# Optimization experiments

Hardware: AMD Instinct MI355X
Metric: run time of the kernel (lower is better)

## Reference

```python
import jax, jax.numpy as jnp
import numpy as np

# Constants derived from quantiles=[0.1..0.9] (deciles), df = 9.
QUANTILES = jnp.array([0.1, 0.2, 0.3, 0.4, 0.5, 0.6, 0.7, 0.8, 0.9], dtype=jnp.float32)
# scipy.stats.norm.ppf(quantiles), cast to float32 as in the torch module
Z_SCORES = jnp.array([-1.2815516, -0.8416212, -0.5244005, -0.2533471, 0.0,
                      0.2533471, 0.5244005, 0.8416212, 1.2815516], dtype=jnp.float32)
# expected bin probabilities: q0, diffs, 1-q_last -> all 0.1 for deciles
EXPECTED_PCT = jnp.full((10,), 0.1, dtype=jnp.float32)
# chi2.ppf(1 - p, df=9) for p in QUANTILES (precomputed with scipy offline)
CRIT = jnp.array([14.683657, 12.242145, 10.656372, 9.413640, 8.342832,
                  7.357034, 6.393306, 5.380053, 4.168159], dtype=jnp.float32)
MAX_CRIT = 14.683657
SHARPNESS = 100.0  # sigmoid steepness for the soft histogram


def setup_inputs() -> dict:
    key = jax.random.key(0)
    x = jax.random.normal(key, (16777216,), dtype=jnp.float32)
    return {"x": x}


def reference(x):
    n = x.shape[0]
    mean = x.mean()
    std = jnp.std(x, ddof=1)  # torch.std uses Bessel's correction
    z = (x - mean) / std  # [n]
    # soft cumulative counts at each quantile threshold: [K]
    cum = jax.nn.sigmoid(SHARPNESS * (Z_SCORES[:, None] - z[None, :])).sum(axis=1)
    # bin counts: first cum, consecutive diffs, remainder n - last cum -> [K+1]
    actual = jnp.concatenate([cum[:1], jnp.diff(cum),
                              jnp.asarray(n, z.dtype)[None] - cum[-1:]])
    expected = n * EXPECTED_PCT
    chi2_stat = jnp.sum((actual - expected) ** 2 / (expected + 1e-7))
    # differentiable interpolation of p-value
    w = jax.nn.softmax(-jnp.abs(chi2_stat - CRIT))
    p_value_estimate = 1.0 - jnp.sum(w * QUANTILES)
    excess = jax.nn.relu((chi2_stat - MAX_CRIT) / 100.0)
    return p_value_estimate + excess
```

## Files before the change

kernel.cpp:

```cpp
#include <hip/hip_runtime.h>
#include <math.h>


#if __has_builtin(__builtin_amdgcn_exp2f)
#define EXP2F(x) __builtin_amdgcn_exp2f(x)
#else
#define EXP2F(x) exp2f(x)
#endif
#if __has_builtin(__builtin_amdgcn_rcpf)
#define RCPF(x) __builtin_amdgcn_rcpf(x)
#else
#define RCPF(x) (1.0f / (x))
#endif

#define NBLK 256
#define ABLOCK 1024
#define NBINS 8192

static __device__ __forceinline__ double wave_reduce_d(double v) {
#pragma unroll
    for (int off = 32; off > 0; off >>= 1) v += __shfl_down(v, off);
    return v;
}

__device__ __constant__ double d_ZS[9] = {
    -1.2815516, -0.8416212, -0.5244005, -0.2533471, 0.0,
    0.2533471,  0.5244005,  0.8416212,  1.2815516};

__device__ void epilogue(const double* cum, float* out, int n) {
    const double CRIT[9] = {14.683657, 12.242145, 10.656372, 9.413640, 8.342832,
                            7.357034,  6.393306,  5.380053,  4.168159};
    const double nd = (double)n;
    double actual[10];
    actual[0] = cum[0];
#pragma unroll
    for (int k = 1; k < 9; ++k) actual[k] = cum[k] - cum[k - 1];
    actual[9] = nd - cum[8];
    const double expected = nd * (double)0.1f;
    const double denom = expected + 1e-7;
    double chi2 = 0.0;
#pragma unroll
    for (int j = 0; j < 10; ++j) {
        double d = actual[j] - expected;
        chi2 += d * d / denom;
    }
    double dneg[9], m = -1e300;
#pragma unroll
    for (int k = 0; k < 9; ++k) {
        dneg[k] = -fabs(chi2 - CRIT[k]);
        if (dneg[k] > m) m = dneg[k];
    }
    double W = 0.0, PQ = 0.0;
#pragma unroll
    for (int k = 0; k < 9; ++k) {
        double w = exp(dneg[k] - m);
        W += w;
        PQ += w * (0.1 * (double)(k + 1));
    }
    double p = 1.0 - PQ / W;
    double excess = (chi2 - 14.683657) / 100.0;
    if (excess < 0.0) excess = 0.0;
    out[0] = (float)(p + excess);
}

__global__ __launch_bounds__(ABLOCK) void init_kernel(unsigned int* __restrict__ H,
                                                      unsigned int* __restrict__ ticket) {
    const int t = blockIdx.x * ABLOCK + threadIdx.x;
    if (t < NBINS) H[t] = 0u;
    if (t == 0) *ticket = 0u;
}

__global__ __launch_bounds__(ABLOCK) void fused_kernel(
    const float* __restrict__ x, double* __restrict__ part1,
    unsigned int* __restrict__ H, unsigned int* __restrict__ ticket,
    float* __restrict__ out, int n) {
    __shared__ unsigned int hist[NBINS];
    __shared__ double smd[16][9];
    __shared__ double sMV[2];
    __shared__ int sLast;
    const int tx = threadIdx.x;
    const int lane = tx & 63, wid = tx >> 6;

#pragma unroll
    for (int j = 0; j < NBINS / ABLOCK; ++j) hist[tx + j * ABLOCK] = 0u;
    __syncthreads();

    float fs = 0.f, fss = 0.f;
    auto process = [&](float v) {
        fs += v;
        fss = fmaf(v, v, fss);
        int b = (int)fmaf(v, 512.0f, 4096.0f);
        b = b < 0 ? 0 : (b > NBINS - 1 ? NBINS - 1 : b);
        atomicAdd(&hist[b], 1u);
    };

    const int tid = blockIdx.x * ABLOCK + tx;
    const int nthreads = NBLK * ABLOCK;
    const int n4 = n >> 2;
    const float4* __restrict__ x4 = (const float4*)x;
    for (int i = tid; i < n4; i += nthreads) {
        float4 v = x4[i];
        process(v.x); process(v.y); process(v.z); process(v.w);
    }
    if (blockIdx.x == 0 && tx == 0) {
        for (int j = n4 << 2; j < n; ++j) process(x[j]);
    }
    __syncthreads();

#pragma unroll
    for (int j = 0; j < NBINS / ABLOCK; ++j) {
        const int jj = (j + (int)blockIdx.x) & (NBINS / ABLOCK - 1);
        const int b = tx + jj * ABLOCK;
        const unsigned int h = hist[b];
        if (h) atomicAdd(&H[b], h);
    }

    double s = wave_reduce_d((double)fs);
    double ss = wave_reduce_d((double)fss);
    if (lane == 0) { smd[wid][0] = s; smd[wid][1] = ss; }
    __syncthreads();
    if (tx == 0) {
        double ts = 0.0, tss = 0.0;
#pragma unroll
        for (int w = 0; w < 16; ++w) { ts += smd[w][0]; tss += smd[w][1]; }
        __hip_atomic_store(&part1[2 * blockIdx.x], ts, __ATOMIC_RELAXED,
                           __HIP_MEMORY_SCOPE_AGENT);
        __hip_atomic_store(&part1[2 * blockIdx.x + 1], tss, __ATOMIC_RELAXED,
                           __HIP_MEMORY_SCOPE_AGENT);
    }

    __syncthreads();
    if (tx == 0) {
        __threadfence();
        const unsigned int prev = __hip_atomic_fetch_add(
            ticket, 1u, __ATOMIC_ACQ_REL, __HIP_MEMORY_SCOPE_AGENT);
        sLast = (prev == (unsigned int)(NBLK - 1));
    }
    __syncthreads();
    if (!sLast) return;
    __threadfence();

    double ps = 0.0, pss = 0.0;
    if (tx < NBLK) {
        ps = __hip_atomic_load(&part1[2 * tx], __ATOMIC_RELAXED,
                               __HIP_MEMORY_SCOPE_AGENT);
        pss = __hip_atomic_load(&part1[2 * tx + 1], __ATOMIC_RELAXED,
                                __HIP_MEMORY_SCOPE_AGENT);
    }
    double rs = wave_reduce_d(ps);
    double rss = wave_reduce_d(pss);
    __syncthreads();
    if (lane == 0) { smd[wid][0] = rs; smd[wid][1] = rss; }
    __syncthreads();
    if (tx == 0) {
        double ts = 0.0, tss = 0.0;
#pragma unroll
        for (int w = 0; w < 16; ++w) { ts += smd[w][0]; tss += smd[w][1]; }
        const double nd = (double)n;
        const double mean = ts / nd;
        const double var = (tss - ts * ts / nd) / (nd - 1.0);
        sMV[0] = mean;
        sMV[1] = 1.0 / sqrt(var);
    }
    __syncthreads();
    const double mu = sMV[0], isig = sMV[1];
    const double Ld = 144.26950408889634;
    const double wz = (1.0 / 512.0) * isig;
    const double wz2_12 = wz * wz / 12.0;
    const double hgl = wz * 0.28867513459481287;

    double acc[9];
#pragma unroll
    for (int k = 0; k < 9; ++k) acc[k] = 0.0;

    for (int b = tx; b < NBINS; b += ABLOCK) {
        const unsigned int h = __hip_atomic_load(&H[b], __ATOMIC_RELAXED,
                                                 __HIP_MEMORY_SCOPE_AGENT);
        if (h == 0u) continue;
        const double dh = (double)h;
        const double c = (double)b * (1.0 / 512.0) + (0.5 / 512.0 - 8.0);
        const double zc = (c - mu) * isig;
        const double zctr = zc - zc * wz2_12;
        const double z1 = zctr - hgl, z2 = zctr + hgl;
#pragma unroll
        for (int k = 0; k < 9; ++k) {
            const float t1 = EXP2F((float)(Ld * (z1 - d_ZS[k])));
            const float t2 = EXP2F((float)(Ld * (z2 - d_ZS[k])));
            const double sg =
                0.5 * ((double)RCPF(1.0f + t1) + (double)RCPF(1.0f + t2));
            acc[k] += dh * sg;
        }
    }

    __syncthreads();
#pragma unroll
    for (int k = 0; k < 9; ++k) {
        double r = wave_reduce_d(acc[k]);
        if (lane == 0) smd[wid][k] = r;
    }
    __syncthreads();
    if (tx == 0) {
        double cum[9];
#pragma unroll
        for (int k = 0; k < 9; ++k) {
            double t = 0.0;
#pragma unroll
            for (int w = 0; w < 16; ++w) t += smd[w][k];
            cum[k] = t;
        }
        epilogue(cum, out, n);
    }
}

extern "C" void kernel_launch(void* const* d_in, const int* in_sizes, int n_in,
                              void* d_out, int out_size, void* d_ws, size_t ws_size,
                              hipStream_t stream) {
    const float* x = (const float*)d_in[0];
    const int n = in_sizes[0];
    double* part1 = (double*)d_ws;
    unsigned int* H = (unsigned int*)(part1 + 512);
    unsigned int* ticket = H + NBINS;

    init_kernel<<<8, ABLOCK, 0, stream>>>(H, ticket);
    fused_kernel<<<NBLK, ABLOCK, 0, stream>>>(x, part1, H, ticket,
                                              (float*)d_out, n);
}
```

Before: 121.9 us.

## Replace global histogram merge with cooperative grid sync and per-block sigmoid evaluation

Launches the kernel cooperatively and uses a grid-wide sync after the mean/variance partials, so every block can evaluate the soft-sigmoid sums on its own shared-memory histogram. This removes the atomic merge into a global histogram, the separate init kernel, and the single last-block tail that evaluated all bins alone. Per-block cumulative sums are written to a second partial buffer and reduced by the last block via a ticket, which is reset inside the kernel. In exchange, every block repeats the bin loop over all 8192 bins, and a cooperative launch and grid barrier are added.

```diff
diff --git a/kernel.cpp b/kernel.cpp
--- a/kernel.cpp
+++ b/kernel.cpp
@@ -1,5 +1,8 @@
 #include <hip/hip_runtime.h>
+#include <hip/hip_cooperative_groups.h>
 #include <math.h>
+
+namespace cg = cooperative_groups;
 
 
 #if __has_builtin(__builtin_amdgcn_exp2f)
@@ -63,23 +66,20 @@
     out[0] = (float)(p + excess);
 }
 
-__global__ __launch_bounds__(ABLOCK) void init_kernel(unsigned int* __restrict__ H,
-                                                      unsigned int* __restrict__ ticket) {
-    const int t = blockIdx.x * ABLOCK + threadIdx.x;
-    if (t < NBINS) H[t] = 0u;
-    if (t == 0) *ticket = 0u;
-}
-
 __global__ __launch_bounds__(ABLOCK) void fused_kernel(
     const float* __restrict__ x, double* __restrict__ part1,
-    unsigned int* __restrict__ H, unsigned int* __restrict__ ticket,
+    double* __restrict__ part2, unsigned int* __restrict__ ticket,
     float* __restrict__ out, int n) {
+    cg::grid_group grid = cg::this_grid();
     __shared__ unsigned int hist[NBINS];
     __shared__ double smd[16][9];
     __shared__ double sMV[2];
     __shared__ int sLast;
     const int tx = threadIdx.x;
     const int lane = tx & 63, wid = tx >> 6;
+
+    if (blockIdx.x == 0 && tx == 0)
+        __hip_atomic_store(ticket, 0u, __ATOMIC_RELAXED, __HIP_MEMORY_SCOPE_AGENT);
 
 #pragma unroll
     for (int j = 0; j < NBINS / ABLOCK; ++j) hist[tx + j * ABLOCK] = 0u;
@@ -107,14 +107,6 @@
     }
     __syncthreads();
 
-#pragma unroll
-    for (int j = 0; j < NBINS / ABLOCK; ++j) {
-        const int jj = (j + (int)blockIdx.x) & (NBINS / ABLOCK - 1);
-        const int b = tx + jj * ABLOCK;
-        const unsigned int h = hist[b];
-        if (h) atomicAdd(&H[b], h);
-    }
-
     double s = wave_reduce_d((double)fs);
     double ss = wave_reduce_d((double)fss);
     if (lane == 0) { smd[wid][0] = s; smd[wid][1] = ss; }
@@ -127,18 +119,10 @@
                            __HIP_MEMORY_SCOPE_AGENT);
         __hip_atomic_store(&part1[2 * blockIdx.x + 1], tss, __ATOMIC_RELAXED,
                            __HIP_MEMORY_SCOPE_AGENT);
-    }
-
-    __syncthreads();
-    if (tx == 0) {
         __threadfence();
-        const unsigned int prev = __hip_atomic_fetch_add(
-            ticket, 1u, __ATOMIC_ACQ_REL, __HIP_MEMORY_SCOPE_AGENT);
-        sLast = (prev == (unsigned int)(NBLK - 1));
-    }
-    __syncthreads();
-    if (!sLast) return;
-    __threadfence();
+    }
+
+    grid.sync();
 
     double ps = 0.0, pss = 0.0;
     if (tx < NBLK) {
@@ -174,8 +158,7 @@
     for (int k = 0; k < 9; ++k) acc[k] = 0.0;
 
     for (int b = tx; b < NBINS; b += ABLOCK) {
-        const unsigned int h = __hip_atomic_load(&H[b], __ATOMIC_RELAXED,
-                                                 __HIP_MEMORY_SCOPE_AGENT);
+        const unsigned int h = hist[b];
         if (h == 0u) continue;
         const double dh = (double)h;
         const double c = (double)b * (1.0 / 512.0) + (0.5 / 512.0 - 8.0);
@@ -200,6 +183,40 @@
     }
     __syncthreads();
     if (tx == 0) {
+#pragma unroll
+        for (int k = 0; k < 9; ++k) {
+            double t = 0.0;
+#pragma unroll
+            for (int w = 0; w < 16; ++w) t += smd[w][k];
+            __hip_atomic_store(&part2[blockIdx.x * 9 + k], t, __ATOMIC_RELAXED,
+                               __HIP_MEMORY_SCOPE_AGENT);
+        }
+        __threadfence();
+        const unsigned int prev = __hip_atomic_fetch_add(
+            ticket, 1u, __ATOMIC_ACQ_REL, __HIP_MEMORY_SCOPE_AGENT);
+        sLast = (prev == (unsigned int)(NBLK - 1));
+    }
+    __syncthreads();
+    if (!sLast) return;
+    __threadfence();
+
+    double v9[9];
+#pragma unroll
+    for (int k = 0; k < 9; ++k) v9[k] = 0.0;
+    if (tx < NBLK) {
+#pragma unroll
+        for (int k = 0; k < 9; ++k)
+            v9[k] = __hip_atomic_load(&part2[tx * 9 + k], __ATOMIC_RELAXED,
+                                      __HIP_MEMORY_SCOPE_AGENT);
+    }
+    __syncthreads();
+#pragma unroll
+    for (int k = 0; k < 9; ++k) {
+        double r = wave_reduce_d(v9[k]);
+        if (lane == 0) smd[wid][k] = r;
+    }
+    __syncthreads();
+    if (tx == 0) {
         double cum[9];
 #pragma unroll
         for (int k = 0; k < 9; ++k) {
@@ -216,12 +233,14 @@
                               void* d_out, int out_size, void* d_ws, size_t ws_size,
                               hipStream_t stream) {
     const float* x = (const float*)d_in[0];
-    const int n = in_sizes[0];
+    int n = in_sizes[0];
     double* part1 = (double*)d_ws;
-    unsigned int* H = (unsigned int*)(part1 + 512);
-    unsigned int* ticket = H + NBINS;
-
-    init_kernel<<<8, ABLOCK, 0, stream>>>(H, ticket);
-    fused_kernel<<<NBLK, ABLOCK, 0, stream>>>(x, part1, H, ticket,
-                                              (float*)d_out, n);
-}
+    double* part2 = part1 + 512;
+    unsigned int* ticket = (unsigned int*)(part2 + NBLK * 9);
+    float* outp = (float*)d_out;
+
+    void* kargs[] = {(void*)&x, (void*)&part1, (void*)&part2,
+                     (void*)&ticket, (void*)&outp, (void*)&n};
+    hipLaunchCooperativeKernel((void*)fused_kernel, dim3(NBLK), dim3(ABLOCK),
+                               kargs, 0u, stream);
+}
```

After: 166.3 us. 1.36x slower.

## Replicate global histogram, double block count, and batch loads per thread

Applied to the files above, without the earlier changes.

Doubles the grid to 512 blocks with a launch-bounds occupancy hint, and unrolls the streaming loop to issue four float4 loads before processing them. The global histogram is split into 8 replicas indexed by block to spread atomic contention, and the last block sums the replicas when reading. In exchange, init and the final reduction touch 8x more histogram memory, and the extra blocks add more shared-histogram flushes.

```diff
diff --git a/kernel.cpp b/kernel.cpp
--- a/kernel.cpp
+++ b/kernel.cpp
@@ -13,9 +13,10 @@
 #define RCPF(x) (1.0f / (x))
 #endif
 
-#define NBLK 256
+#define NBLK 512
 #define ABLOCK 1024
 #define NBINS 8192
+#define NREP 8
 
 static __device__ __forceinline__ double wave_reduce_d(double v) {
 #pragma unroll
@@ -66,11 +67,11 @@
 __global__ __launch_bounds__(ABLOCK) void init_kernel(unsigned int* __restrict__ H,
                                                       unsigned int* __restrict__ ticket) {
     const int t = blockIdx.x * ABLOCK + threadIdx.x;
-    if (t < NBINS) H[t] = 0u;
+    if (t < NREP * NBINS) H[t] = 0u;
     if (t == 0) *ticket = 0u;
 }
 
-__global__ __launch_bounds__(ABLOCK) void fused_kernel(
+__global__ __launch_bounds__(ABLOCK, 8) void fused_kernel(
     const float* __restrict__ x, double* __restrict__ part1,
     unsigned int* __restrict__ H, unsigned int* __restrict__ ticket,
     float* __restrict__ out, int n) {
@@ -93,26 +94,35 @@
         b = b < 0 ? 0 : (b > NBINS - 1 ? NBINS - 1 : b);
         atomicAdd(&hist[b], 1u);
     };
+    auto process4 = [&](float4 v) {
+        process(v.x); process(v.y); process(v.z); process(v.w);
+    };
 
     const int tid = blockIdx.x * ABLOCK + tx;
-    const int nthreads = NBLK * ABLOCK;
+    const int NT = NBLK * ABLOCK;
     const int n4 = n >> 2;
     const float4* __restrict__ x4 = (const float4*)x;
-    for (int i = tid; i < n4; i += nthreads) {
-        float4 v = x4[i];
-        process(v.x); process(v.y); process(v.z); process(v.w);
-    }
+    int i = tid;
+    for (; i + 3 * NT < n4; i += 4 * NT) {
+        float4 v0 = x4[i];
+        float4 v1 = x4[i + NT];
+        float4 v2 = x4[i + 2 * NT];
+        float4 v3 = x4[i + 3 * NT];
+        process4(v0); process4(v1); process4(v2); process4(v3);
+    }
+    for (; i < n4; i += NT) process4(x4[i]);
     if (blockIdx.x == 0 && tx == 0) {
         for (int j = n4 << 2; j < n; ++j) process(x[j]);
     }
     __syncthreads();
 
+    unsigned int* __restrict__ Hr = H + (blockIdx.x & (NREP - 1)) * NBINS;
 #pragma unroll
     for (int j = 0; j < NBINS / ABLOCK; ++j) {
-        const int jj = (j + (int)blockIdx.x) & (NBINS / ABLOCK - 1);
+        const int jj = (j + (int)(blockIdx.x >> 3)) & (NBINS / ABLOCK - 1);
         const int b = tx + jj * ABLOCK;
         const unsigned int h = hist[b];
-        if (h) atomicAdd(&H[b], h);
+        if (h) atomicAdd(&Hr[b], h);
     }
 
     double s = wave_reduce_d((double)fs);
@@ -174,8 +184,11 @@
     for (int k = 0; k < 9; ++k) acc[k] = 0.0;
 
     for (int b = tx; b < NBINS; b += ABLOCK) {
-        const unsigned int h = __hip_atomic_load(&H[b], __ATOMIC_RELAXED,
-                                                 __HIP_MEMORY_SCOPE_AGENT);
+        unsigned int h = 0u;
+#pragma unroll
+        for (int r = 0; r < NREP; ++r)
+            h += __hip_atomic_load(&H[r * NBINS + b], __ATOMIC_RELAXED,
+                                   __HIP_MEMORY_SCOPE_AGENT);
         if (h == 0u) continue;
         const double dh = (double)h;
         const double c = (double)b * (1.0 / 512.0) + (0.5 / 512.0 - 8.0);
@@ -218,10 +231,10 @@
     const float* x = (const float*)d_in[0];
     const int n = in_sizes[0];
     double* part1 = (double*)d_ws;
-    unsigned int* H = (unsigned int*)(part1 + 512);
-    unsigned int* ticket = H + NBINS;
-
-    init_kernel<<<8, ABLOCK, 0, stream>>>(H, ticket);
+    unsigned int* H = (unsigned int*)(part1 + 2 * NBLK);
+    unsigned int* ticket = H + NREP * NBINS;
+
+    init_kernel<<<64, ABLOCK, 0, stream>>>(H, ticket);
     fused_kernel<<<NBLK, ABLOCK, 0, stream>>>(x, part1, H, ticket,
                                               (float*)d_out, n);
 }
```

After: 142.3 us. +16.7%, slower.
